# Kernel tuning notes

Measured on AMD Instinct MI355X. Metric: run time of the kernel, lower is better.

## Reference

```python
import jax, jax.numpy as jnp
import numpy as np

B, S = 1024, 200
NUM_ITEMS = 1000000
PQ_M = 8
VALS = 256
SUB_DIM = 16  # embedding_size (128) // pq_m (8)


def setup_inputs() -> dict:
    key = jax.random.key(0)
    k1, k2, k3 = jax.random.split(key, 3)
    input_ids = jax.random.randint(k1, (B, S), 0, NUM_ITEMS, dtype=jnp.int64)
    # item_codes buffer has num_items + 2 rows (padding/mask rows), byte codes in [0, 256)
    item_codes = jax.random.randint(k2, (NUM_ITEMS + 2, PQ_M), 0, VALS, dtype=jnp.int32)
    # centroids ~ U(-0.05, 0.05) as in nn.init.uniform_
    centroids = jax.random.uniform(k3, (PQ_M, VALS, SUB_DIM), dtype=jnp.float32,
                                   minval=-0.05, maxval=0.05)
    return {"input_ids": input_ids, "item_codes": item_codes, "centroids": centroids}


def reference(input_ids, item_codes, centroids):
    # input_codes: [B, S, PQ_M] byte codes for each item in the sequence
    codes = item_codes[input_ids]
    # Per-byte embedding lookup: centroids[dim, codes[..., dim]] for each dim,
    # vectorized as a single fancy gather -> [B, S, PQ_M, SUB_DIM]
    dim_idx = jnp.arange(centroids.shape[0])[None, None, :]  # [1, 1, PQ_M]
    sub_emb = centroids[dim_idx, codes]
    # torch.cat of per-dim sub-embeddings along last dim == reshape
    return sub_emb.reshape(codes.shape[0], codes.shape[1], -1)  # [B, S, 128]
```

## Files before the change

kernel.cpp:

```cpp
#include <hip/hip_runtime.h>
#include <hip/hip_bf16.h>

#define BB 1024
#define SS 200
#define PQ_M 8
#define VALS 256
#define SUB_DIM 16
#define N_TOKENS (BB * SS)
#define OUT_PER_TOKEN (PQ_M * SUB_DIM)

#define T_PER_THREAD 4
#define TOK_SLICE (N_TOKENS / T_PER_THREAD)

__global__ __launch_bounds__(256) void pq_gather_kernel(
    const int*   __restrict__ ids,
    const int*   __restrict__ codes,
    const float* __restrict__ cent,
    float*       __restrict__ out)
{
    const int gid  = blockIdx.x * blockDim.x + threadIdx.x;
    const int t    = gid & 31;
    const int slot = gid >> 5;
    const int m    = t >> 2;
    const int c4   = t & 3;

    int tok[T_PER_THREAD];
#pragma unroll
    for (int j = 0; j < T_PER_THREAD; ++j)
        tok[j] = slot + j * TOK_SLICE;

    int id[T_PER_THREAD];
#pragma unroll
    for (int j = 0; j < T_PER_THREAD; ++j)
        id[j] = ids[tok[j]];

    int code[T_PER_THREAD];
#pragma unroll
    for (int j = 0; j < T_PER_THREAD; ++j)
        code[j] = codes[id[j] * PQ_M + m];

    float4 v[T_PER_THREAD];
    const float4* cent4 = (const float4*)cent;
#pragma unroll
    for (int j = 0; j < T_PER_THREAD; ++j)
        v[j] = cent4[(m * VALS + code[j]) * (SUB_DIM / 4) + c4];

#pragma unroll
    for (int j = 0; j < T_PER_THREAD; ++j)
        ((float4*)(out + (size_t)tok[j] * OUT_PER_TOKEN))[t] = v[j];
}

extern "C" void kernel_launch(void* const* d_in, const int* in_sizes, int n_in,
                              void* d_out, int out_size, void* d_ws, size_t ws_size,
                              hipStream_t stream)
{
    const int*   ids   = (const int*)d_in[0];
    const int*   codes = (const int*)d_in[1];
    const float* cent  = (const float*)d_in[2];
    float*       out   = (float*)d_out;

    const int total_threads = (N_TOKENS / T_PER_THREAD) * 32;
    const int block = 256;
    const int grid  = total_threads / block;
    pq_gather_kernel<<<grid, block, 0, stream>>>(ids, codes, cent, out);
}
```

Baseline: 143.9 us.

## Split gather into code-packing pass and centroid expansion with nontemporal stores

Adds a first kernel that gathers each token's 8 int32 codes with vectorized loads and packs them into one 64-bit word in workspace. A second kernel reads that packed word and expands it into centroid rows, writing the output with nontemporal stores. Previously each of 32 threads per token issued its own dependent id load and a scattered code load. The split replaces that duplicated random traffic with one coalesced packed read, at the cost of an extra launch and a workspace round trip. The old single kernel is kept as a fallback when the workspace is missing or too small.

```diff
diff --git a/kernel.cpp b/kernel.cpp
--- a/kernel.cpp
+++ b/kernel.cpp
@@ -1,5 +1,4 @@
 #include <hip/hip_runtime.h>
-#include <hip/hip_bf16.h>
 
 #define BB 1024
 #define SS 200
@@ -9,8 +8,60 @@
 #define N_TOKENS (BB * SS)
 #define OUT_PER_TOKEN (PQ_M * SUB_DIM)
 
+typedef float f32x4 __attribute__((ext_vector_type(4)));
+typedef int   i32x4 __attribute__((ext_vector_type(4)));
+
+__global__ __launch_bounds__(256) void gather_codes_kernel(
+    const int*    __restrict__ ids,
+    const i32x4*  __restrict__ codes4,
+    unsigned int* __restrict__ packed)
+{
+    const int gid  = blockIdx.x * blockDim.x + threadIdx.x;
+    const int half = gid & 1;
+    const int tok  = gid >> 1;
+
+    const int id = ids[tok];
+    const i32x4 c = codes4[(size_t)id * 2 + half];
+
+    const unsigned int p = (unsigned int)(c.x & 255)
+                         | ((unsigned int)(c.y & 255) << 8)
+                         | ((unsigned int)(c.z & 255) << 16)
+                         | ((unsigned int)(c.w & 255) << 24);
+    packed[gid] = p;
+}
+
 #define T_PER_THREAD 4
 #define TOK_SLICE (N_TOKENS / T_PER_THREAD)
+
+__global__ __launch_bounds__(256) void expand_kernel(
+    const unsigned long long* __restrict__ packed,
+    const f32x4* __restrict__ cent4,
+    float*       __restrict__ out)
+{
+    const int gid  = blockIdx.x * blockDim.x + threadIdx.x;
+    const int t    = gid & 31;
+    const int slot = gid >> 5;
+    const int m    = t >> 2;
+    const int c4   = t & 3;
+
+    unsigned long long p[T_PER_THREAD];
+#pragma unroll
+    for (int j = 0; j < T_PER_THREAD; ++j)
+        p[j] = packed[slot + j * TOK_SLICE];
+
+    f32x4 v[T_PER_THREAD];
+#pragma unroll
+    for (int j = 0; j < T_PER_THREAD; ++j) {
+        const int code = (int)((p[j] >> (8 * m)) & 255ULL);
+        v[j] = cent4[(m * VALS + code) * (SUB_DIM / 4) + c4];
+    }
+
+#pragma unroll
+    for (int j = 0; j < T_PER_THREAD; ++j) {
+        f32x4* dst = (f32x4*)(out + (size_t)(slot + j * TOK_SLICE) * OUT_PER_TOKEN);
+        __builtin_nontemporal_store(v[j], dst + t);
+    }
+}
 
 __global__ __launch_bounds__(256) void pq_gather_kernel(
     const int*   __restrict__ ids,
@@ -59,8 +110,19 @@
     const float* cent  = (const float*)d_in[2];
     float*       out   = (float*)d_out;
 
-    const int total_threads = (N_TOKENS / T_PER_THREAD) * 32;
-    const int block = 256;
-    const int grid  = total_threads / block;
-    pq_gather_kernel<<<grid, block, 0, stream>>>(ids, codes, cent, out);
+    const size_t packed_bytes = (size_t)N_TOKENS * 8;
+
+    if (d_ws != nullptr && ws_size >= packed_bytes) {
+        unsigned int* packed = (unsigned int*)d_ws;
+
+        gather_codes_kernel<<<(N_TOKENS * 2) / 256, 256, 0, stream>>>(
+            ids, (const i32x4*)codes, packed);
+
+        expand_kernel<<<(N_TOKENS / T_PER_THREAD) * 32 / 256, 256, 0, stream>>>(
+            (const unsigned long long*)packed, (const f32x4*)cent, out);
+    } else {
+        const int total_threads = (N_TOKENS / T_PER_THREAD) * 32;
+        pq_gather_kernel<<<total_threads / 256, 256, 0, stream>>>(
+            ids, codes, cent, out);
+    }
 }
```

Result: faster. 139.9 us (-2.7%).

## Stage packed per-token codes in shared memory and use nontemporal output stores

Applied to the files above, without the earlier changes.

Each block now handles 128 contiguous tokens. Two threads per token load that token's 8 codes as two 16-byte vectors, pack them into bytes and place them in shared memory. Warps then read codes from LDS to gather centroid rows and write the output with nontemporal stores. This replaces the eight redundant scalar code loads per token with vector loads, and keeps the large streaming output from polluting cache. The cost is an added barrier and shared-memory staging, and each thread now handles sixteen tokens instead of four.

```diff
diff --git a/kernel.cpp b/kernel.cpp
--- a/kernel.cpp
+++ b/kernel.cpp
@@ -1,5 +1,4 @@
 #include <hip/hip_runtime.h>
-#include <hip/hip_bf16.h>
 
 #define BB 1024
 #define SS 200
@@ -9,45 +8,50 @@
 #define N_TOKENS (BB * SS)
 #define OUT_PER_TOKEN (PQ_M * SUB_DIM)
 
-#define T_PER_THREAD 4
-#define TOK_SLICE (N_TOKENS / T_PER_THREAD)
+typedef float f32x4 __attribute__((ext_vector_type(4)));
+typedef int   i32x4 __attribute__((ext_vector_type(4)));
 
-__global__ __launch_bounds__(256) void pq_gather_kernel(
+#define TOK_PER_BLOCK 128
+#define BLOCK_THREADS 256
+
+__global__ __launch_bounds__(BLOCK_THREADS) void pq_fused_kernel(
     const int*   __restrict__ ids,
-    const int*   __restrict__ codes,
-    const float* __restrict__ cent,
+    const i32x4* __restrict__ codes4,
+    const f32x4* __restrict__ cent4,
     float*       __restrict__ out)
 {
-    const int gid  = blockIdx.x * blockDim.x + threadIdx.x;
-    const int t    = gid & 31;
-    const int slot = gid >> 5;
-    const int m    = t >> 2;
-    const int c4   = t & 3;
+    __shared__ unsigned int sc[TOK_PER_BLOCK * 2];
 
-    int tok[T_PER_THREAD];
-#pragma unroll
-    for (int j = 0; j < T_PER_THREAD; ++j)
-        tok[j] = slot + j * TOK_SLICE;
+    const int base = blockIdx.x * TOK_PER_BLOCK;
+    const int tid  = threadIdx.x;
 
-    int id[T_PER_THREAD];
-#pragma unroll
-    for (int j = 0; j < T_PER_THREAD; ++j)
-        id[j] = ids[tok[j]];
+    {
+        const int tok  = tid >> 1;
+        const int half = tid & 1;
+        const int id   = ids[base + tok];
+        const i32x4 c  = codes4[(size_t)id * 2 + half];
+        sc[tok * 2 + half] = (unsigned int)(c.x & 255)
+                           | ((unsigned int)(c.y & 255) << 8)
+                           | ((unsigned int)(c.z & 255) << 16)
+                           | ((unsigned int)(c.w & 255) << 24);
+    }
+    __syncthreads();
 
-    int code[T_PER_THREAD];
-#pragma unroll
-    for (int j = 0; j < T_PER_THREAD; ++j)
-        code[j] = codes[id[j] * PQ_M + m];
-
-    float4 v[T_PER_THREAD];
-    const float4* cent4 = (const float4*)cent;
-#pragma unroll
-    for (int j = 0; j < T_PER_THREAD; ++j)
-        v[j] = cent4[(m * VALS + code[j]) * (SUB_DIM / 4) + c4];
+    const int t   = tid & 31;
+    const int grp = tid >> 5;
+    const int m   = t >> 2;
+    const int c4  = t & 3;
+    const int w   = m >> 2;
+    const int sh  = 8 * (m & 3);
 
 #pragma unroll
-    for (int j = 0; j < T_PER_THREAD; ++j)
-        ((float4*)(out + (size_t)tok[j] * OUT_PER_TOKEN))[t] = v[j];
+    for (int i = 0; i < TOK_PER_BLOCK / 8; ++i) {
+        const int tok  = i * 8 + grp;
+        const int code = (int)((sc[tok * 2 + w] >> sh) & 255u);
+        const f32x4 v  = cent4[(m * VALS + code) * (SUB_DIM / 4) + c4];
+        f32x4* dst = (f32x4*)(out + (size_t)(base + tok) * OUT_PER_TOKEN);
+        __builtin_nontemporal_store(v, dst + t);
+    }
 }
 
 extern "C" void kernel_launch(void* const* d_in, const int* in_sizes, int n_in,
@@ -59,8 +63,7 @@
     const float* cent  = (const float*)d_in[2];
     float*       out   = (float*)d_out;
 
-    const int total_threads = (N_TOKENS / T_PER_THREAD) * 32;
-    const int block = 256;
-    const int grid  = total_threads / block;
-    pq_gather_kernel<<<grid, block, 0, stream>>>(ids, codes, cent, out);
+    const int grid = N_TOKENS / TOK_PER_BLOCK;
+    pq_fused_kernel<<<grid, BLOCK_THREADS, 0, stream>>>(
+        ids, (const i32x4*)codes, (const f32x4*)cent, out);
 }
```

Measured after the change: 141.5 us. No clear change (-1.6%).
